# Kernel optimization log

Hardware: AMD Instinct MI355X
Metric: run time of the kernel (lower is better)

## Reference

```python
import jax, jax.numpy as jnp
import numpy as np

B, N, DIM = 2, 2048, 512
H = 8
DH = DIM // H
ALPHA = 1.0
DELTA = 1.0
EPS = 1e-5


def setup_inputs() -> dict:
    key = jax.random.key(0)
    ks = jax.random.split(key, 5)
    scale = 0.02
    return {
        "z": jax.random.normal(ks[0], (B, N, DIM), dtype=jnp.float32),
        "Wq": jax.random.normal(ks[1], (DIM, DIM), dtype=jnp.float32) * scale,
        "bq": jnp.zeros((DIM,), dtype=jnp.float32),
        "Wk": jax.random.normal(ks[2], (DIM, DIM), dtype=jnp.float32) * scale,
        "bk": jnp.zeros((DIM,), dtype=jnp.float32),
        "Wv": jax.random.normal(ks[3], (DIM, DIM), dtype=jnp.float32) * scale,
        "bv": jnp.zeros((DIM,), dtype=jnp.float32),
        "Wo": jax.random.normal(ks[4], (DIM, DIM), dtype=jnp.float32) * scale,
        "bo": jnp.zeros((DIM,), dtype=jnp.float32),
    }


def _split_heads(x):
    # [B, N, DIM] -> [B, H, N, DH]
    b, n, _ = x.shape
    return x.reshape(b, n, H, DH).transpose(0, 2, 1, 3)


def reference(z, Wq, bq, Wk, bk, Wv, bv, Wo, bo):
    Q = _split_heads(z @ Wq + bq)
    K = _split_heads(z @ Wk + bk)
    V = _split_heads(z @ Wv + bv)

    # QK^T once; reuse for both the score and the squared-distance expansion
    qk = jnp.einsum("bhnd,bhmd->bhnm", Q, K)  # [B,H,N,N]

    # NeuroFocal deviation NF(Q): per-query scalar
    mu_q = Q.mean(axis=-1, keepdims=True)
    var_q = ((Q - mu_q) ** 2).mean(axis=-1, keepdims=True)
    sigma_q = jnp.sqrt(var_q + EPS)
    nf_q = jnp.abs(Q - mu_q).sum(axis=-1, keepdims=True) / (sigma_q + EPS)  # [B,H,N,1]

    # ||Q - K||^2 = |Q|^2 + |K|^2 - 2 QK^T (same math as explicit diff tensor)
    q2 = (Q ** 2).sum(axis=-1)  # [B,H,N]
    k2 = (K ** 2).sum(axis=-1)  # [B,H,N]
    omega = q2[..., :, None] + k2[..., None, :] - 2.0 * qk  # [B,H,N,N]
    omega = omega / (jnp.exp(-DELTA * nf_q) + 1.0)

    logits = qk / jnp.sqrt(jnp.float32(DH)) - ALPHA * omega
    A = jax.nn.softmax(logits, axis=-1)

    out = jnp.einsum("bhnm,bhmd->bhnd", A, V)  # [B,H,N,DH]
    out = out.transpose(0, 2, 1, 3).reshape(z.shape[0], z.shape[1], DIM)
    return out @ Wo + bo
```

## Files before the change

kernel.cpp:

```cpp
#include <hip/hip_runtime.h>
#include <hip/hip_bf16.h>

#define HH 8
#define NNq 2048
#define EPSF 1e-5f
#define LOG2E 1.4426950408889634f

typedef __bf16 bf16x8 __attribute__((ext_vector_type(8)));
typedef float f32x4 __attribute__((ext_vector_type(4)));

typedef const __attribute__((address_space(1))) unsigned int* gas_t;
typedef __attribute__((address_space(3))) unsigned int* las_t;

__device__ __forceinline__ void async16(const void* g, void* l) {
  __builtin_amdgcn_global_load_lds((gas_t)g, (las_t)l, 16, 0, 0);
}
__device__ __forceinline__ void async4(const void* g, void* l) {
  __builtin_amdgcn_global_load_lds((gas_t)g, (las_t)l, 4, 0, 0);
}

__device__ __forceinline__ unsigned short f2bf(float f) {
  union { float f; unsigned int u; } a;
  a.f = f;
  unsigned int r = a.u + 0x7fffu + ((a.u >> 16) & 1u);
  return (unsigned short)(r >> 16);
}

__global__ __launch_bounds__(256) void convert_z(const float* __restrict__ z,
                                                 unsigned short* __restrict__ zb) {
  const int i = (blockIdx.x * 256 + threadIdx.x) * 8;
  const float4 a = *(const float4*)&z[i];
  const float4 b = *(const float4*)&z[i + 4];
  union { unsigned short us[8]; uint4 v; } o;
  o.us[0] = f2bf(a.x); o.us[1] = f2bf(a.y); o.us[2] = f2bf(a.z); o.us[3] = f2bf(a.w);
  o.us[4] = f2bf(b.x); o.us[5] = f2bf(b.y); o.us[6] = f2bf(b.z); o.us[7] = f2bf(b.w);
  *(uint4*)&zb[i] = o.v;
}

__global__ __launch_bounds__(256) void transw_kernel(
    const float* __restrict__ W0, const float* __restrict__ W1,
    const float* __restrict__ W2, const float* __restrict__ W3,
    unsigned short* __restrict__ Wt) {
  __shared__ float Tl[64][68];
  const float* W = (blockIdx.z == 0) ? W0 : (blockIdx.z == 1) ? W1
                   : (blockIdx.z == 2) ? W2 : W3;
  unsigned short* dst = Wt + (size_t)blockIdx.z * 262144;
  const int t = threadIdx.x;
  const int k0 = blockIdx.x * 64, n0 = blockIdx.y * 64;
#pragma unroll
  for (int i = 0; i < 4; ++i) {
    const int idx = t + 256 * i;
    const int row = idx >> 4, cq = (idx & 15) * 4;
    *(float4*)&Tl[row][cq] = *(const float4*)&W[(size_t)(k0 + row) * 512 + n0 + cq];
  }
  __syncthreads();
#pragma unroll
  for (int i = 0; i < 4; ++i) {
    const int idx = t + 256 * i;
    const int nr = idx >> 4, kq = (idx & 15) * 4;
    ushort4 o;
    o.x = f2bf(Tl[kq + 0][nr]);
    o.y = f2bf(Tl[kq + 1][nr]);
    o.z = f2bf(Tl[kq + 2][nr]);
    o.w = f2bf(Tl[kq + 3][nr]);
    *(ushort4*)&dst[(size_t)(n0 + nr) * 512 + k0 + kq] = o;
  }
}

__global__ __launch_bounds__(256) void gemm_qkv(
    const unsigned short* __restrict__ A, const unsigned short* __restrict__ Wt3,
    const float* __restrict__ bq, const float* __restrict__ bk,
    const float* __restrict__ bvv, unsigned short* __restrict__ Qb,
    unsigned short* __restrict__ Ksw, unsigned short* __restrict__ Vsw,
    float* __restrict__ c1a, float* __restrict__ dva, float* __restrict__ k2a,
    float* __restrict__ q2a, unsigned int* __restrict__ k2max) {
  __shared__ __align__(16) unsigned short S[12288];
  __shared__ float wmax[4];

  const int which = blockIdx.z;
  const unsigned short* Wt = Wt3 + (size_t)which * 262144;
  const float* bias = (which == 0) ? bq : (which == 1) ? bk : bvv;

  const int t = threadIdx.x;
  const int w = t >> 6, lane = t & 63, ln = lane & 15, quad = lane >> 4;
  const int r0 = blockIdx.x * 128, h = blockIdx.y;
  const int c0 = h * 64;
  const int b = r0 >> 11, n0 = r0 & 2047;
  const int bh = b * HH + h;

  f32x4 acc[2][4];
#pragma unroll
  for (int rf = 0; rf < 2; ++rf)
#pragma unroll
    for (int nt = 0; nt < 4; ++nt) acc[rf][nt] = (f32x4)(0.0f);

  const int lr = lane >> 3, lc = (lane & 7) * 8;

  for (int k0 = 0; k0 < 512; k0 += 64) {
#pragma unroll
    for (int i = 0; i < 4; ++i)
      async16(A + (size_t)(r0 + w * 32 + i * 8 + lr) * 512 + k0 + lc,
              S + (w * 32 + i * 8) * 64);
#pragma unroll
    for (int i = 0; i < 2; ++i)
      async16(Wt + (size_t)(c0 + w * 16 + i * 8 + lr) * 512 + k0 + lc,
              S + 8192 + (w * 16 + i * 8) * 64);
    __syncthreads();
#pragma unroll
    for (int kk = 0; kk < 64; kk += 32) {
      bf16x8 af[2];
#pragma unroll
      for (int rf = 0; rf < 2; ++rf)
        af[rf] = *(const bf16x8*)&S[(w * 32 + rf * 16 + ln) * 64 + kk + quad * 8];
#pragma unroll
      for (int nt = 0; nt < 4; ++nt) {
        const bf16x8 bf = *(const bf16x8*)&S[8192 + (nt * 16 + ln) * 64 + kk + quad * 8];
#pragma unroll
        for (int rf = 0; rf < 2; ++rf)
          acc[rf][nt] = __builtin_amdgcn_mfma_f32_16x16x32_bf16(af[rf], bf, acc[rf][nt], 0, 0, 0);
      }
    }
    __syncthreads();
  }

  float x[2][4][4];
#pragma unroll
  for (int nt = 0; nt < 4; ++nt) {
    const float bv = bias[c0 + nt * 16 + ln];
#pragma unroll
    for (int rf = 0; rf < 2; ++rf)
#pragma unroll
      for (int r = 0; r < 4; ++r) x[rf][nt][r] = acc[rf][nt][r] + bv;
  }

  if (which == 0) {
#pragma unroll
    for (int rf = 0; rf < 2; ++rf)
#pragma unroll
      for (int r = 0; r < 4; ++r) {
        float s1 = x[rf][0][r] + x[rf][1][r] + x[rf][2][r] + x[rf][3][r];
#pragma unroll
        for (int off = 1; off < 16; off <<= 1) s1 += __shfl_xor(s1, off, 64);
        const float mu = s1 * (1.0f / 64.0f);
        float s2 = 0.0f, sa = 0.0f;
#pragma unroll
        for (int nt = 0; nt < 4; ++nt) {
          const float dx = x[rf][nt][r] - mu;
          s2 += dx * dx;
          sa += fabsf(dx);
        }
#pragma unroll
        for (int off = 1; off < 16; off <<= 1) {
          s2 += __shfl_xor(s2, off, 64);
          sa += __shfl_xor(sa, off, 64);
        }
        if (ln == 0) {
          const float sigma = sqrtf(s2 * (1.0f / 64.0f) + EPSF);
          const float nf = sa / (sigma + EPSF);
          const float dInv = 1.0f / (__expf(-nf) + 1.0f);
          const int row = bh * NNq + n0 + w * 32 + rf * 16 + quad * 4 + r;
          c1a[row] = (0.125f + 2.0f * dInv) * LOG2E;
          dva[row] = dInv * LOG2E;
          q2a[row] = s2 + 64.0f * mu * mu;
        }
      }
#pragma unroll
    for (int rf = 0; rf < 2; ++rf)
#pragma unroll
      for (int nt = 0; nt < 4; ++nt)
#pragma unroll
        for (int r = 0; r < 4; ++r)
          S[(w * 32 + rf * 16 + quad * 4 + r) * 72 + nt * 16 + ln] = f2bf(x[rf][nt][r]);
    __syncthreads();
#pragma unroll
    for (int i = 0; i < 4; ++i) {
      const int idx = t + 256 * i;
      const int q = idx >> 3, c = idx & 7;
      *(uint4*)&Qb[((size_t)bh * NNq + n0 + q) * 64 + c * 8] =
          *(const uint4*)&S[q * 72 + c * 8];
    }
  } else if (which == 1) {
    float mx = 0.0f;
#pragma unroll
    for (int rf = 0; rf < 2; ++rf)
#pragma unroll
      for (int r = 0; r < 4; ++r) {
        float s2 = 0.0f;
#pragma unroll
        for (int nt = 0; nt < 4; ++nt) s2 += x[rf][nt][r] * x[rf][nt][r];
#pragma unroll
        for (int off = 1; off < 16; off <<= 1) s2 += __shfl_xor(s2, off, 64);
        if (ln == 0) k2a[bh * NNq + n0 + w * 32 + rf * 16 + quad * 4 + r] = s2;
        mx = fmaxf(mx, s2);
      }
#pragma unroll
    for (int off = 16; off < 64; off <<= 1) mx = fmaxf(mx, __shfl_xor(mx, off, 64));
    if (lane == 0) wmax[w] = mx;
#pragma unroll
    for (int rf = 0; rf < 2; ++rf)
#pragma unroll
      for (int nt = 0; nt < 4; ++nt) {
        const int c = nt * 2 + (ln >> 3);
#pragma unroll
        for (int r = 0; r < 4; ++r) {
          const int key = w * 32 + rf * 16 + quad * 4 + r;
          const int klo = key & 63;
          S[(key >> 6) * 4096 + klo * 64 + ((c ^ (klo & 7)) * 8) + (ln & 7)] =
              f2bf(x[rf][nt][r]);
        }
      }
    __syncthreads();
    if (t == 0) {
      const float m = fmaxf(fmaxf(wmax[0], wmax[1]), fmaxf(wmax[2], wmax[3]));
      atomicMax(&k2max[bh * 16], __float_as_uint(m));
    }
    unsigned short* dst = Ksw + ((size_t)bh * 32 + (n0 >> 6)) * 4096;
#pragma unroll
    for (int i = 0; i < 4; ++i) {
      const int idx = t + 256 * i;
      *(uint4*)&dst[idx * 8] = *(const uint4*)&S[idx * 8];
    }
  } else {
#pragma unroll
    for (int rf = 0; rf < 2; ++rf)
#pragma unroll
      for (int nt = 0; nt < 4; ++nt) {
        const int d = nt * 16 + ln;
#pragma unroll
        for (int r = 0; r < 4; ++r) {
          const int key = w * 32 + rf * 16 + quad * 4 + r;
          const int klo = key & 63;
          S[d * 128 + (key >> 6) * 64 + (((klo >> 3) ^ (d & 7)) * 8) + (klo & 7)] =
              f2bf(x[rf][nt][r]);
        }
      }
    __syncthreads();
    unsigned short* dst = Vsw + ((size_t)bh * 32 + (n0 >> 6)) * 4096;
#pragma unroll
    for (int i = 0; i < 4; ++i) {
      const int g = t + 256 * i;
      const int tile = g >> 9, d = (g >> 3) & 63, j8 = (g & 7) * 8;
      *(uint4*)&dst[tile * 4096 + d * 64 + j8] =
          *(const uint4*)&S[d * 128 + tile * 64 + j8];
    }
  }
}

__global__ __launch_bounds__(256) void attn_kernel(
    const unsigned short* __restrict__ Qb, const unsigned short* __restrict__ Ksw,
    const unsigned short* __restrict__ Vsw, const float* __restrict__ c1a,
    const float* __restrict__ dva, const float* __restrict__ k2a,
    const float* __restrict__ q2a, const unsigned int* __restrict__ k2maxu,
    unsigned short* __restrict__ attnb) {
  __shared__ __align__(16) unsigned short Kt[4096];
  __shared__ __align__(16) unsigned short Vt[4096];
  __shared__ __align__(16) unsigned short Ps[64 * 72];
  __shared__ __align__(16) float k2t[64];

  const int t = threadIdx.x;
  const int w = t >> 6, lane = t & 63, ln = lane & 15, quad = lane >> 4;
  const int qt = blockIdx.x, bh = blockIdx.y;
  const int b = bh >> 3, h = bh & 7;
  const int q0 = qt * 64;
  const int rowbase = bh * NNq;

  const int qg = q0 + w * 16 + ln;
  const unsigned short* qrow = Qb + ((size_t)rowbase + qg) * 64;
  const bf16x8 aq0 = *(const bf16x8*)(qrow + quad * 8);
  const bf16x8 aq1 = *(const bf16x8*)(qrow + 32 + quad * 8);

  const float k2m = __uint_as_float(k2maxu[bh * 16]);
  const float c1q = c1a[rowbase + qg];
  const float dvq = dva[rowbase + qg];
  const float Mqq = c1q * sqrtf(q2a[rowbase + qg] * k2m);
  float L = 0.0f;
  f32x4 O[4];
#pragma unroll
  for (int nt = 0; nt < 4; ++nt) O[nt] = (f32x4)(0.0f);

  const unsigned short* Kg = Ksw + (size_t)bh * 32 * 4096;
  const unsigned short* Vg = Vsw + (size_t)bh * 32 * 4096;
  const float* k2g = k2a + rowbase;
  const int sw = quad ^ (ln & 7);
  const int sw1 = (4 + quad) ^ (ln & 7);

  for (int kt = 0; kt < 32; ++kt) {
    {
      const size_t tb = (size_t)kt * 4096 + w * 1024;
      async16(Kg + tb + lane * 8, Kt + w * 1024);
      async16(Kg + tb + 512 + lane * 8, Kt + w * 1024 + 512);
      async16(Vg + tb + lane * 8, Vt + w * 1024);
      async16(Vg + tb + 512 + lane * 8, Vt + w * 1024 + 512);
      if (w == 0) async4(k2g + kt * 64 + lane, k2t);
    }
    __syncthreads();

    f32x4 s[4];
#pragma unroll
    for (int nt = 0; nt < 4; ++nt) {
      const unsigned short* kb = Kt + (nt * 16 + ln) * 64;
      const bf16x8 b0 = *(const bf16x8*)(kb + sw * 8);
      const bf16x8 b1 = *(const bf16x8*)(kb + sw1 * 8);
      f32x4 a = (f32x4)(0.0f);
      a = __builtin_amdgcn_mfma_f32_16x16x32_bf16(b0, aq0, a, 0, 0, 0);
      a = __builtin_amdgcn_mfma_f32_16x16x32_bf16(b1, aq1, a, 0, 0, 0);
      s[nt] = a;
    }

#pragma unroll
    for (int nt = 0; nt < 4; ++nt) {
      const f32x4 k2v = *(const f32x4*)&k2t[nt * 16 + quad * 4];
      ushort4 pk;
      float p0 = __builtin_amdgcn_exp2f(c1q * s[nt][0] - dvq * k2v[0] - Mqq);
      float p1 = __builtin_amdgcn_exp2f(c1q * s[nt][1] - dvq * k2v[1] - Mqq);
      float p2 = __builtin_amdgcn_exp2f(c1q * s[nt][2] - dvq * k2v[2] - Mqq);
      float p3 = __builtin_amdgcn_exp2f(c1q * s[nt][3] - dvq * k2v[3] - Mqq);
      L += (p0 + p1) + (p2 + p3);
      pk.x = f2bf(p0); pk.y = f2bf(p1); pk.z = f2bf(p2); pk.w = f2bf(p3);
      *(ushort4*)&Ps[(w * 16 + ln) * 72 + nt * 16 + quad * 4] = pk;
    }
    const unsigned short* pr = Ps + (w * 16 + ln) * 72;
    const bf16x8 pa0 = *(const bf16x8*)(pr + quad * 8);
    const bf16x8 pa1 = *(const bf16x8*)(pr + 32 + quad * 8);

#pragma unroll
    for (int nt = 0; nt < 4; ++nt) {
      const unsigned short* vb = Vt + (nt * 16 + ln) * 64;
      const bf16x8 vb0 = *(const bf16x8*)(vb + sw * 8);
      const bf16x8 vb1 = *(const bf16x8*)(vb + sw1 * 8);
      O[nt] = __builtin_amdgcn_mfma_f32_16x16x32_bf16(pa0, vb0, O[nt], 0, 0, 0);
      O[nt] = __builtin_amdgcn_mfma_f32_16x16x32_bf16(pa1, vb1, O[nt], 0, 0, 0);
    }
    __syncthreads();
  }

  L += __shfl_xor(L, 16, 64);
  L += __shfl_xor(L, 32, 64);
  float inv[4];
#pragma unroll
  for (int r = 0; r < 4; ++r) {
    const float Lr = __shfl(L, quad * 4 + r, 64);
    inv[r] = 1.0f / Lr;
  }
#pragma unroll
  for (int nt = 0; nt < 4; ++nt)
#pragma unroll
    for (int r = 0; r < 4; ++r)
      Ps[(w * 16 + quad * 4 + r) * 72 + nt * 16 + ln] = f2bf(O[nt][r] * inv[r]);
  __syncthreads();
#pragma unroll
  for (int i = 0; i < 2; ++i) {
    const int idx = t + 256 * i;
    const int q = idx >> 3, c = idx & 7;
    *(uint4*)&attnb[((size_t)(b * NNq + q0 + q)) * 512 + h * 64 + c * 8] =
        *(const uint4*)&Ps[q * 72 + c * 8];
  }
}

__global__ __launch_bounds__(256) void gemm_out(
    const unsigned short* __restrict__ A, const unsigned short* __restrict__ Wt,
    const float* __restrict__ bias, float* __restrict__ of) {
  __shared__ __align__(16) unsigned short S[8192];
  __shared__ float Tl[64][68];
  const int t = threadIdx.x;
  const int w = t >> 6, lane = t & 63, ln = lane & 15, quad = lane >> 4;
  const int r0 = blockIdx.x * 64, c0 = blockIdx.y * 64;
  const int lr = lane >> 3, lc = (lane & 7) * 8;

  f32x4 acc[4];
#pragma unroll
  for (int nt = 0; nt < 4; ++nt) acc[nt] = (f32x4)(0.0f);

  for (int k0 = 0; k0 < 512; k0 += 64) {
#pragma unroll
    for (int i = 0; i < 2; ++i) {
      async16(A + (size_t)(r0 + w * 16 + i * 8 + lr) * 512 + k0 + lc,
              S + (w * 16 + i * 8) * 64);
      async16(Wt + (size_t)(c0 + w * 16 + i * 8 + lr) * 512 + k0 + lc,
              S + 4096 + (w * 16 + i * 8) * 64);
    }
    __syncthreads();
#pragma unroll
    for (int kk = 0; kk < 64; kk += 32) {
      const bf16x8 af = *(const bf16x8*)&S[(w * 16 + ln) * 64 + kk + quad * 8];
#pragma unroll
      for (int nt = 0; nt < 4; ++nt) {
        const bf16x8 bf = *(const bf16x8*)&S[4096 + (nt * 16 + ln) * 64 + kk + quad * 8];
        acc[nt] = __builtin_amdgcn_mfma_f32_16x16x32_bf16(af, bf, acc[nt], 0, 0, 0);
      }
    }
    __syncthreads();
  }
#pragma unroll
  for (int nt = 0; nt < 4; ++nt) {
    const float bv = bias[c0 + nt * 16 + ln];
#pragma unroll
    for (int r = 0; r < 4; ++r)
      Tl[w * 16 + quad * 4 + r][nt * 16 + ln] = acc[nt][r] + bv;
  }
  __syncthreads();
#pragma unroll
  for (int i = 0; i < 4; ++i) {
    const int idx = t + 256 * i;
    const int row = idx >> 4, c4 = (idx & 15) * 4;
    *(float4*)&of[(size_t)(r0 + row) * 512 + c0 + c4] = *(const float4*)&Tl[row][c4];
  }
}

extern "C" void kernel_launch(void* const* d_in, const int* in_sizes, int n_in,
                              void* d_out, int out_size, void* d_ws,
                              size_t ws_size, hipStream_t stream) {
  const float* z = (const float*)d_in[0];
  const float* Wq = (const float*)d_in[1];
  const float* bq = (const float*)d_in[2];
  const float* Wk = (const float*)d_in[3];
  const float* bk = (const float*)d_in[4];
  const float* Wv = (const float*)d_in[5];
  const float* bv = (const float*)d_in[6];
  const float* Wo = (const float*)d_in[7];
  const float* bo = (const float*)d_in[8];
  float* out = (float*)d_out;

  char* ws = (char*)d_ws;
  unsigned short* zb = (unsigned short*)(ws);
  unsigned short* Wt = (unsigned short*)(ws + 4194304);
  unsigned short* Qb = (unsigned short*)(ws + 6291456);
  unsigned short* Ksw = (unsigned short*)(ws + 10485760);
  unsigned short* Vsw = (unsigned short*)(ws + 14680064);
  float* c1 = (float*)(ws + 18874368);
  float* dv = (float*)(ws + 19005440);
  float* k2 = (float*)(ws + 19136512);
  float* q2 = (float*)(ws + 19267584);
  unsigned short* attnb = (unsigned short*)(ws + 19398656);
  unsigned int* k2max = (unsigned int*)(ws + 23592960);

  hipLaunchKernelGGL(convert_z, dim3(1024), dim3(256), 0, stream, z, zb);
  hipLaunchKernelGGL(transw_kernel, dim3(8, 8, 4), dim3(256), 0, stream,
                     Wq, Wk, Wv, Wo, Wt);
  hipMemsetAsync(k2max, 0, 1024, stream);
  hipLaunchKernelGGL(gemm_qkv, dim3(32, 8, 3), dim3(256), 0, stream, zb, Wt,
                     bq, bk, bv, Qb, Ksw, Vsw, c1, dv, k2, q2, k2max);
  hipLaunchKernelGGL(attn_kernel, dim3(32, 16), dim3(256), 0, stream, Qb, Ksw,
                     Vsw, c1, dv, k2, q2, k2max, attnb);
  hipLaunchKernelGGL(gemm_out, dim3(64, 8), dim3(256), 0, stream, attnb,
                     Wt + 786432, bo, out);
}
```

Before: 148.7 us.

## Split attention key range across two wave groups and fuse prep kernels

The attention kernel now launches 512 threads per block, and the two halves each process half of the key tiles into separate shared-memory buffers. Their partial outputs and row sums are combined through shared memory at the end, which doubles the waves per block to improve latency hiding over the 512 blocks. Separately, the z conversion, weight transpose and k2max memset are merged into one launch to cut launch overhead. This costs more shared memory per block, which may limit occupancy, and adds a cross-half reduction step.

```diff
diff --git a/kernel.cpp b/kernel.cpp
--- a/kernel.cpp
+++ b/kernel.cpp
@@ -26,44 +26,48 @@
   return (unsigned short)(r >> 16);
 }
 
-__global__ __launch_bounds__(256) void convert_z(const float* __restrict__ z,
-                                                 unsigned short* __restrict__ zb) {
-  const int i = (blockIdx.x * 256 + threadIdx.x) * 8;
-  const float4 a = *(const float4*)&z[i];
-  const float4 b = *(const float4*)&z[i + 4];
-  union { unsigned short us[8]; uint4 v; } o;
-  o.us[0] = f2bf(a.x); o.us[1] = f2bf(a.y); o.us[2] = f2bf(a.z); o.us[3] = f2bf(a.w);
-  o.us[4] = f2bf(b.x); o.us[5] = f2bf(b.y); o.us[6] = f2bf(b.z); o.us[7] = f2bf(b.w);
-  *(uint4*)&zb[i] = o.v;
-}
-
-__global__ __launch_bounds__(256) void transw_kernel(
-    const float* __restrict__ W0, const float* __restrict__ W1,
-    const float* __restrict__ W2, const float* __restrict__ W3,
-    unsigned short* __restrict__ Wt) {
+__global__ __launch_bounds__(256) void prep_kernel(
+    const float* __restrict__ z, const float* __restrict__ W0,
+    const float* __restrict__ W1, const float* __restrict__ W2,
+    const float* __restrict__ W3, unsigned short* __restrict__ zb,
+    unsigned short* __restrict__ Wt, unsigned int* __restrict__ k2max) {
   __shared__ float Tl[64][68];
-  const float* W = (blockIdx.z == 0) ? W0 : (blockIdx.z == 1) ? W1
-                   : (blockIdx.z == 2) ? W2 : W3;
-  unsigned short* dst = Wt + (size_t)blockIdx.z * 262144;
   const int t = threadIdx.x;
-  const int k0 = blockIdx.x * 64, n0 = blockIdx.y * 64;
-#pragma unroll
-  for (int i = 0; i < 4; ++i) {
-    const int idx = t + 256 * i;
-    const int row = idx >> 4, cq = (idx & 15) * 4;
-    *(float4*)&Tl[row][cq] = *(const float4*)&W[(size_t)(k0 + row) * 512 + n0 + cq];
-  }
-  __syncthreads();
-#pragma unroll
-  for (int i = 0; i < 4; ++i) {
-    const int idx = t + 256 * i;
-    const int nr = idx >> 4, kq = (idx & 15) * 4;
-    ushort4 o;
-    o.x = f2bf(Tl[kq + 0][nr]);
-    o.y = f2bf(Tl[kq + 1][nr]);
-    o.z = f2bf(Tl[kq + 2][nr]);
-    o.w = f2bf(Tl[kq + 3][nr]);
-    *(ushort4*)&dst[(size_t)(n0 + nr) * 512 + k0 + kq] = o;
+  const int bx = blockIdx.x;
+  if (bx < 1024) {
+    const int i = (bx * 256 + t) * 8;
+    const float4 a = *(const float4*)&z[i];
+    const float4 b = *(const float4*)&z[i + 4];
+    union { unsigned short us[8]; uint4 v; } o;
+    o.us[0] = f2bf(a.x); o.us[1] = f2bf(a.y); o.us[2] = f2bf(a.z); o.us[3] = f2bf(a.w);
+    o.us[4] = f2bf(b.x); o.us[5] = f2bf(b.y); o.us[6] = f2bf(b.z); o.us[7] = f2bf(b.w);
+    *(uint4*)&zb[i] = o.v;
+  } else if (bx < 1280) {
+    const int idx0 = bx - 1024;
+    const int wsel = idx0 >> 6, rem = idx0 & 63;
+    const int k0 = (rem >> 3) * 64, n0 = (rem & 7) * 64;
+    const float* W = (wsel == 0) ? W0 : (wsel == 1) ? W1 : (wsel == 2) ? W2 : W3;
+    unsigned short* dst = Wt + (size_t)wsel * 262144;
+#pragma unroll
+    for (int i = 0; i < 4; ++i) {
+      const int idx = t + 256 * i;
+      const int row = idx >> 4, cq = (idx & 15) * 4;
+      *(float4*)&Tl[row][cq] = *(const float4*)&W[(size_t)(k0 + row) * 512 + n0 + cq];
+    }
+    __syncthreads();
+#pragma unroll
+    for (int i = 0; i < 4; ++i) {
+      const int idx = t + 256 * i;
+      const int nr = idx >> 4, kq = (idx & 15) * 4;
+      ushort4 o;
+      o.x = f2bf(Tl[kq + 0][nr]);
+      o.y = f2bf(Tl[kq + 1][nr]);
+      o.z = f2bf(Tl[kq + 2][nr]);
+      o.w = f2bf(Tl[kq + 3][nr]);
+      *(ushort4*)&dst[(size_t)(n0 + nr) * 512 + k0 + kq] = o;
+    }
+  } else {
+    k2max[t] = 0u;
   }
 }
 
@@ -246,25 +250,28 @@
   }
 }
 
-__global__ __launch_bounds__(256) void attn_kernel(
+__global__ __launch_bounds__(512) void attn_kernel(
     const unsigned short* __restrict__ Qb, const unsigned short* __restrict__ Ksw,
     const unsigned short* __restrict__ Vsw, const float* __restrict__ c1a,
     const float* __restrict__ dva, const float* __restrict__ k2a,
     const float* __restrict__ q2a, const unsigned int* __restrict__ k2maxu,
     unsigned short* __restrict__ attnb) {
-  __shared__ __align__(16) unsigned short Kt[4096];
-  __shared__ __align__(16) unsigned short Vt[4096];
-  __shared__ __align__(16) unsigned short Ps[64 * 72];
-  __shared__ __align__(16) float k2t[64];
+  __shared__ __align__(16) char smem[51712];
 
   const int t = threadIdx.x;
-  const int w = t >> 6, lane = t & 63, ln = lane & 15, quad = lane >> 4;
+  const int w8 = t >> 6, lane = t & 63, ln = lane & 15, quad = lane >> 4;
+  const int half = w8 >> 2, wl = w8 & 3;
   const int qt = blockIdx.x, bh = blockIdx.y;
   const int b = bh >> 3, h = bh & 7;
   const int q0 = qt * 64;
   const int rowbase = bh * NNq;
 
-  const int qg = q0 + w * 16 + ln;
+  unsigned short* Kt = (unsigned short*)(smem + half * 16384);
+  unsigned short* Vt = (unsigned short*)(smem + half * 16384 + 8192);
+  unsigned short* Ps = (unsigned short*)(smem + 32768 + half * 9216);
+  float* k2t = (float*)(smem + 51200 + half * 256);
+
+  const int qg = q0 + wl * 16 + ln;
   const unsigned short* qrow = Qb + ((size_t)rowbase + qg) * 64;
   const bf16x8 aq0 = *(const bf16x8*)(qrow + quad * 8);
   const bf16x8 aq1 = *(const bf16x8*)(qrow + 32 + quad * 8);
@@ -280,18 +287,18 @@
 
   const unsigned short* Kg = Ksw + (size_t)bh * 32 * 4096;
   const unsigned short* Vg = Vsw + (size_t)bh * 32 * 4096;
-  const float* k2g = k2a + rowbase;
+  const float* k2g = k2a + rowbase + half * 1024;
   const int sw = quad ^ (ln & 7);
   const int sw1 = (4 + quad) ^ (ln & 7);
 
-  for (int kt = 0; kt < 32; ++kt) {
+  for (int kt = 0; kt < 16; ++kt) {
     {
-      const size_t tb = (size_t)kt * 4096 + w * 1024;
-      async16(Kg + tb + lane * 8, Kt + w * 1024);
-      async16(Kg + tb + 512 + lane * 8, Kt + w * 1024 + 512);
-      async16(Vg + tb + lane * 8, Vt + w * 1024);
-      async16(Vg + tb + 512 + lane * 8, Vt + w * 1024 + 512);
-      if (w == 0) async4(k2g + kt * 64 + lane, k2t);
+      const size_t tb = (size_t)(half * 16 + kt) * 4096 + wl * 1024;
+      async16(Kg + tb + lane * 8, Kt + wl * 1024);
+      async16(Kg + tb + 512 + lane * 8, Kt + wl * 1024 + 512);
+      async16(Vg + tb + lane * 8, Vt + wl * 1024);
+      async16(Vg + tb + 512 + lane * 8, Vt + wl * 1024 + 512);
+      if (wl == 0) async4(k2g + kt * 64 + lane, k2t);
     }
     __syncthreads();
 
@@ -317,9 +324,9 @@
       float p3 = __builtin_amdgcn_exp2f(c1q * s[nt][3] - dvq * k2v[3] - Mqq);
       L += (p0 + p1) + (p2 + p3);
       pk.x = f2bf(p0); pk.y = f2bf(p1); pk.z = f2bf(p2); pk.w = f2bf(p3);
-      *(ushort4*)&Ps[(w * 16 + ln) * 72 + nt * 16 + quad * 4] = pk;
-    }
-    const unsigned short* pr = Ps + (w * 16 + ln) * 72;
+      *(ushort4*)&Ps[(wl * 16 + ln) * 72 + nt * 16 + quad * 4] = pk;
+    }
+    const unsigned short* pr = Ps + (wl * 16 + ln) * 72;
     const bf16x8 pa0 = *(const bf16x8*)(pr + quad * 8);
     const bf16x8 pa1 = *(const bf16x8*)(pr + 32 + quad * 8);
 
@@ -336,25 +343,38 @@
 
   L += __shfl_xor(L, 16, 64);
   L += __shfl_xor(L, 32, 64);
-  float inv[4];
-#pragma unroll
-  for (int r = 0; r < 4; ++r) {
-    const float Lr = __shfl(L, quad * 4 + r, 64);
-    inv[r] = 1.0f / Lr;
-  }
+
+  float* Ost = (float*)(smem + half * 16384);
+  float* Lst = (float*)(smem + 32768 + half * 9216);
 #pragma unroll
   for (int nt = 0; nt < 4; ++nt)
 #pragma unroll
     for (int r = 0; r < 4; ++r)
-      Ps[(w * 16 + quad * 4 + r) * 72 + nt * 16 + ln] = f2bf(O[nt][r] * inv[r]);
+      Ost[(wl * 16 + quad * 4 + r) * 64 + nt * 16 + ln] = O[nt][r];
+  if (quad == 0) Lst[wl * 16 + ln] = L;
   __syncthreads();
-#pragma unroll
-  for (int i = 0; i < 2; ++i) {
-    const int idx = t + 256 * i;
-    const int q = idx >> 3, c = idx & 7;
-    *(uint4*)&attnb[((size_t)(b * NNq + q0 + q)) * 512 + h * 64 + c * 8] =
-        *(const uint4*)&Ps[q * 72 + c * 8];
-  }
+
+  const float* O0 = (const float*)smem;
+  const float* O1 = (const float*)(smem + 16384);
+  const float* L0 = (const float*)(smem + 32768);
+  const float* L1 = (const float*)(smem + 32768 + 9216);
+  const int q = t >> 3, c8 = (t & 7) * 8;
+  const float inv = 1.0f / (L0[q] + L1[q]);
+  const int base = q * 64 + c8;
+  float4 a0 = *(const float4*)&O0[base];
+  float4 a1 = *(const float4*)&O0[base + 4];
+  const float4 b0 = *(const float4*)&O1[base];
+  const float4 b1 = *(const float4*)&O1[base + 4];
+  union { unsigned short us[8]; uint4 v; } ov;
+  ov.us[0] = f2bf((a0.x + b0.x) * inv);
+  ov.us[1] = f2bf((a0.y + b0.y) * inv);
+  ov.us[2] = f2bf((a0.z + b0.z) * inv);
+  ov.us[3] = f2bf((a0.w + b0.w) * inv);
+  ov.us[4] = f2bf((a1.x + b1.x) * inv);
+  ov.us[5] = f2bf((a1.y + b1.y) * inv);
+  ov.us[6] = f2bf((a1.z + b1.z) * inv);
+  ov.us[7] = f2bf((a1.w + b1.w) * inv);
+  *(uint4*)&attnb[((size_t)(b * NNq + q0 + q)) * 512 + h * 64 + c8] = ov.v;
 }
 
 __global__ __launch_bounds__(256) void gemm_out(
@@ -434,13 +454,11 @@
   unsigned short* attnb = (unsigned short*)(ws + 19398656);
   unsigned int* k2max = (unsigned int*)(ws + 23592960);
 
-  hipLaunchKernelGGL(convert_z, dim3(1024), dim3(256), 0, stream, z, zb);
-  hipLaunchKernelGGL(transw_kernel, dim3(8, 8, 4), dim3(256), 0, stream,
-                     Wq, Wk, Wv, Wo, Wt);
-  hipMemsetAsync(k2max, 0, 1024, stream);
+  hipLaunchKernelGGL(prep_kernel, dim3(1281), dim3(256), 0, stream, z, Wq, Wk,
+                     Wv, Wo, zb, Wt, k2max);
   hipLaunchKernelGGL(gemm_qkv, dim3(32, 8, 3), dim3(256), 0, stream, zb, Wt,
                      bq, bk, bv, Qb, Ksw, Vsw, c1, dv, k2, q2, k2max);
-  hipLaunchKernelGGL(attn_kernel, dim3(32, 16), dim3(256), 0, stream, Qb, Ksw,
+  hipLaunchKernelGGL(attn_kernel, dim3(32, 16), dim3(512), 0, stream, Qb, Ksw,
                      Vsw, c1, dv, k2, q2, k2max, attnb);
   hipLaunchKernelGGL(gemm_out, dim3(64, 8), dim3(256), 0, stream, attnb,
                      Wt + 786432, bo, out);
```

Result: faster. 142.4 us (-4.2%).
